# Performance work log

Measured on AMD Instinct MI355X. Metric: run time of the kernel, lower is better.

## Reference

```python
import jax, jax.numpy as jnp
import numpy as np
from jax import lax

GROUP = 4  # rt_group_size, reflection=False


def build_weights(W):
    """Symmetrize per GConv3d.get_weight (mid layer, no reflection, no Hermitian).
    W: (O, 1, I, G, kY, kX, kT) -> (O*G, I*G, kY, kX, kT).
    Each group copy k is the previous copy rotated 90 deg in the (kY, kX) plane
    followed by a cyclic shift (+1) along the input-group axis.
    """
    base = W[:, 0]  # (O, I, G, kY, kX, kT)
    ws = [base]
    for _ in range(1, GROUP):
        r = jnp.rot90(ws[-1], k=1, axes=(-3, -2))
        ws.append(jnp.roll(r, shift=1, axis=2))  # cat([last, :-1]) on group axis
    w = jnp.stack(ws, axis=1)  # (O, G, I, G, kY, kX, kT)
    O, _, I, _, kY, kX, kT = w.shape
    return w.reshape(O * GROUP, I * GROUP, kY, kX, kT)


def setup_inputs() -> dict:
    key = jax.random.key(0)
    k1, k2, k3 = jax.random.split(key, 3)
    in_ch, out_ch, k, kT = 16, 16, 3, 3
    x = jax.random.normal(k1, (4, in_ch * GROUP, 32, 64, 64), dtype=jnp.float32)
    # kaiming-ish scale: fan_in = in_ch * GROUP * k * k * kT
    scale = 1.0 / np.sqrt(in_ch * GROUP * k * k * kT)
    W = jax.random.normal(k2, (out_ch, 1, in_ch, GROUP, k, k, kT), dtype=jnp.float32) * scale
    B = jax.random.normal(k3, (1, out_ch, 1, 1, 1), dtype=jnp.float32) * scale
    return {"x": x, "W": W, "B": B}


def reference(x, W, B):
    w = build_weights(W)  # (O*G, I*G, kY, kX, kT)
    y = lax.conv_general_dilated(
        x, w, window_strides=(1, 1, 1), padding='VALID',
        dimension_numbers=('NCDHW', 'OIDHW', 'NCDHW'))
    bias = jnp.repeat(B, GROUP, axis=1)  # repeat_interleave along channel dim
    return y + bias
```

## Files before the change

### kernel.cpp

```cpp
#include <hip/hip_runtime.h>
#include <hip/hip_bf16.h>


typedef __attribute__((ext_vector_type(8))) short bf16x8;
typedef __attribute__((ext_vector_type(4))) float f32x4;

__device__ __forceinline__ void gl_lds16(const void* g, void* l) {
    __builtin_amdgcn_global_load_lds(
        (const __attribute__((address_space(1))) unsigned int*)g,
        (__attribute__((address_space(3))) unsigned int*)l, 16, 0, 0);
}

__global__ __launch_bounds__(256) void build_wT(const float* __restrict__ W,
                                                __hip_bfloat16* __restrict__ wT) {
    int idx = blockIdx.x * 256 + threadIdx.x;
    if (idx >= 27 * 64 * 64) return;
    int ic = idx & 63;
    int oc = (idx >> 6) & 63;
    int tap = idx >> 12;
    int kt = tap % 3, kx = (tap / 3) % 3, ky = tap / 9;
    int o = oc >> 2, kc = oc & 3, i = ic >> 2, gs = ic & 3;
    int sy = ky, sx = kx;
    for (int t = 0; t < kc; ++t) {
        int ny = sx, nx = 2 - sy;
        sy = ny; sx = nx;
        gs = (gs + 3) & 3;
    }
    wT[idx] = __float2bfloat16(W[((o * 16 + i) * 4 + gs) * 27 + sy * 9 + sx * 3 + kt]);
}

__device__ __forceinline__ unsigned int pack2(float a, float b) {
    union { __hip_bfloat162 h2; unsigned int u; } c;
    c.h2 = __hip_bfloat162{__float2bfloat16(a), __float2bfloat16(b)};
    return c.u;
}

__global__ __launch_bounds__(256) void transpose_x(const float* __restrict__ x,
                                                   __hip_bfloat16* __restrict__ xT) {
    __shared__ unsigned int ls[64 * 37];
    int bid = blockIdx.x;
    int hq = bid & 7, d = (bid >> 3) & 31, nb = bid >> 8;
    int tid = threadIdx.x;
    int w4 = tid & 15;
    int kp = tid >> 4;

    for (int hi = 0; hi < 8; ++hi) {
        int h = hq * 8 + hi;
        float4 v0[2], v1[2];
#pragma unroll
        for (int r = 0; r < 2; ++r) {
            int p = r * 16 + kp;
            const float* src = x + ((((size_t)nb * 64 + 2 * p) * 32 + d) * 64 + h) * 64 + w4 * 4;
            v0[r] = *(const float4*)(src);
            v1[r] = *(const float4*)(src + 32 * 64 * 64);
        }
        __syncthreads();
#pragma unroll
        for (int r = 0; r < 2; ++r) {
            int p = r * 16 + kp;
            ls[(w4 * 4 + 0) * 37 + p] = pack2(v0[r].x, v1[r].x);
            ls[(w4 * 4 + 1) * 37 + p] = pack2(v0[r].y, v1[r].y);
            ls[(w4 * 4 + 2) * 37 + p] = pack2(v0[r].z, v1[r].z);
            ls[(w4 * 4 + 3) * 37 + p] = pack2(v0[r].w, v1[r].w);
        }
        __syncthreads();
        __hip_bfloat16* obase = xT + (((size_t)nb * 32 + d) * 64 + h) * 4096;
#pragma unroll
        for (int c = tid; c < 512; c += 256) {
            int ww = c >> 3, icc = c & 7;
            const unsigned int* q = ls + ww * 37 + icc * 4;
            uint4 v;
            v.x = q[0]; v.y = q[1]; v.z = q[2]; v.w = q[3];
            *(uint4*)(obase + ww * 64 + icc * 8) = v;
        }
    }
}

__global__ __launch_bounds__(256, 2) void conv_mfma(const __hip_bfloat16* __restrict__ xT,
                                                    const __hip_bfloat16* __restrict__ wT,
                                                    const float* __restrict__ Bp,
                                                    float* __restrict__ out) {
    __shared__ __align__(16) short sB[6 * 4096 + 128];
    __shared__ __align__(16) short sA[2 * 4096];

    int orig = blockIdx.x;
    int bid = (orig & 7) * 240 + (orig >> 3);
    int ht = bid % 16;
    int d  = (bid / 16) % 30;
    int nb = bid / 480;
    int h0 = ht * 4;

    int tid = threadIdx.x;
    int w = tid >> 6;
    int lane = tid & 63;
    int quad = lane >> 4, col = lane & 15;

    f32x4 acc[4][4];
#pragma unroll
    for (int mt = 0; mt < 4; ++mt)
#pragma unroll
        for (int nt = 0; nt < 4; ++nt) acc[mt][nt] = (f32x4)(0.0f);

    int srcl = ((lane >> 3) << 6) + (((lane & 7) ^ (lane >> 3)) << 3);

    const __hip_bfloat16* xb = xT + (size_t)nb * 8388608 + (size_t)d * 262144;

#pragma unroll
    for (int i = 0; i < 2; ++i) {
        int p = w * 2 + i;
        gl_lds16(wT + p * 512 + srcl, (char*)sA + p * 1024);
    }

    for (int ky = 0; ky < 3; ++ky) {
#pragma unroll
        for (int i = 0; i < 12; ++i) {
            int p = w + i * 4;
            int hh = h0 + (p >> 3);
            if (hh > 63) hh = 63;
            gl_lds16(xb + (size_t)ky * 262144 + hh * 4096 + (p & 7) * 512 + srcl,
                     (char*)sB + p * 1024);
        }
        __syncthreads();

#pragma unroll
        for (int t = 0; t < 9; ++t) {
            {
                const __hip_bfloat16* asrc = wT + (ky * 9 + t + 1) * 4096 + srcl;
                char* adst = (char*)sA + (((ky * 9 + t + 1) & 1) ? 8192 : 0);
#pragma unroll
                for (int i = 0; i < 2; ++i) {
                    int p = w * 2 + i;
                    gl_lds16(asrc + p * 512, adst + p * 1024);
                }
            }

            const int kt = t % 3, kx = t / 3;
            const short* aBase = sA + ((ky * 9 + t) & 1) * 4096;
            int wc = col + kt;
            const short* pb = sB + ((w + kx) * 64 + wc) * 64;
            int bswz = (quad * 8) ^ ((wc & 7) << 3);

#pragma unroll
            for (int ich = 0; ich < 2; ++ich) {
                bf16x8 af[4], bfr[4];
#pragma unroll
                for (int mt = 0; mt < 4; ++mt)
                    af[mt] = *(const bf16x8*)(aBase + col * 64 + mt * 1024
                                              + (((ich * 4 + quad) ^ (col & 7)) << 3));
#pragma unroll
                for (int nt = 0; nt < 4; ++nt)
                    bfr[nt] = *(const bf16x8*)(pb + ((ich * 32) ^ bswz) + nt * 1024);

                __builtin_amdgcn_s_setprio(1);
#pragma unroll
                for (int mt = 0; mt < 4; ++mt)
#pragma unroll
                    for (int nt = 0; nt < 4; ++nt)
                        acc[mt][nt] = __builtin_amdgcn_mfma_f32_16x16x32_bf16(
                            af[mt], bfr[nt], acc[mt][nt], 0, 0, 0);
                __builtin_amdgcn_s_setprio(0);
            }

            __syncthreads();
        }
    }

    int hrow = h0 + w;
    if (hrow < 62) {
#pragma unroll
        for (int mt = 0; mt < 4; ++mt) {
            float bias = Bp[mt * 4 + quad];
#pragma unroll
            for (int nt = 0; nt < 4; ++nt) {
                int wp = nt * 16 + col;
                if (wp < 62) {
#pragma unroll
                    for (int r = 0; r < 4; ++r) {
                        int oc = mt * 16 + quad * 4 + r;
                        out[(((size_t)nb * 64 + oc) * 30 + d) * 3844 + hrow * 62 + wp]
                            = acc[mt][nt][r] + bias;
                    }
                }
            }
        }
    }
}

extern "C" void kernel_launch(void* const* d_in, const int* in_sizes, int n_in,
                              void* d_out, int out_size, void* d_ws, size_t ws_size,
                              hipStream_t stream) {
    const float* x = (const float*)d_in[0];
    const float* W = (const float*)d_in[1];
    const float* Bp = (const float*)d_in[2];
    float* out = (float*)d_out;

    char* ws = (char*)d_ws;
    __hip_bfloat16* wT = (__hip_bfloat16*)ws;
    __hip_bfloat16* xT = (__hip_bfloat16*)(ws + 262144);

    build_wT<<<(27 * 64 * 64 + 255) / 256, 256, 0, stream>>>(W, wT);
    transpose_x<<<4 * 32 * 8, 256, 0, stream>>>(x, xT);
    conv_mfma<<<4 * 30 * 16, 256, 0, stream>>>(xT, wT, Bp, out);
}
```

Measured before the change: 338.0 us.

## Double-buffer input slabs in LDS, stream weights to registers, prefetch transpose rows

The conv kernel now keeps two LDS input slabs. It prefetches the next ky slab during the current ky's taps, spread over the first six taps, and drops the per-tap block barriers. Weight fragments are loaded straight from global memory into registers one tap ahead instead of being staged in LDS. The transpose kernel gets a three-slot register pipeline that loads rows two iterations ahead to overlap global reads with LDS packing. The cost is doubled LDS use, which caps the conv kernel at one block per CU (launch bounds lowered to 1), plus more register pressure and weight reads that rely on the cache hierarchy.

```diff
diff --git a/kernel.cpp b/kernel.cpp
--- a/kernel.cpp
+++ b/kernel.cpp
@@ -44,27 +44,33 @@
     int w4 = tid & 15;
     int kp = tid >> 4;
 
+    float4 a[3][2], b[3][2];
+#define LOADROW(s, hh) do {                                                          \
+    const float* s0_ = x + ((((size_t)nb * 64 + 2 * kp) * 32 + d) * 64 + (hh)) * 64 + w4 * 4;        \
+    const float* s1_ = x + ((((size_t)nb * 64 + 2 * (16 + kp)) * 32 + d) * 64 + (hh)) * 64 + w4 * 4; \
+    a[s][0] = *(const float4*)s0_; b[s][0] = *(const float4*)(s0_ + 131072);         \
+    a[s][1] = *(const float4*)s1_; b[s][1] = *(const float4*)(s1_ + 131072);         \
+} while (0)
+
+    LOADROW(0, hq * 8 + 0);
+    LOADROW(1, hq * 8 + 1);
+#pragma unroll
     for (int hi = 0; hi < 8; ++hi) {
-        int h = hq * 8 + hi;
-        float4 v0[2], v1[2];
+        const int sc = hi % 3, sn = (hi + 2) % 3;
+        asm volatile("s_waitcnt lgkmcnt(0)" ::: "memory");
+        __builtin_amdgcn_s_barrier();
+        if (hi < 6) LOADROW(sn, hq * 8 + hi + 2);
 #pragma unroll
         for (int r = 0; r < 2; ++r) {
             int p = r * 16 + kp;
-            const float* src = x + ((((size_t)nb * 64 + 2 * p) * 32 + d) * 64 + h) * 64 + w4 * 4;
-            v0[r] = *(const float4*)(src);
-            v1[r] = *(const float4*)(src + 32 * 64 * 64);
-        }
-        __syncthreads();
-#pragma unroll
-        for (int r = 0; r < 2; ++r) {
-            int p = r * 16 + kp;
-            ls[(w4 * 4 + 0) * 37 + p] = pack2(v0[r].x, v1[r].x);
-            ls[(w4 * 4 + 1) * 37 + p] = pack2(v0[r].y, v1[r].y);
-            ls[(w4 * 4 + 2) * 37 + p] = pack2(v0[r].z, v1[r].z);
-            ls[(w4 * 4 + 3) * 37 + p] = pack2(v0[r].w, v1[r].w);
-        }
-        __syncthreads();
-        __hip_bfloat16* obase = xT + (((size_t)nb * 32 + d) * 64 + h) * 4096;
+            ls[(w4 * 4 + 0) * 37 + p] = pack2(a[sc][r].x, b[sc][r].x);
+            ls[(w4 * 4 + 1) * 37 + p] = pack2(a[sc][r].y, b[sc][r].y);
+            ls[(w4 * 4 + 2) * 37 + p] = pack2(a[sc][r].z, b[sc][r].z);
+            ls[(w4 * 4 + 3) * 37 + p] = pack2(a[sc][r].w, b[sc][r].w);
+        }
+        asm volatile("s_waitcnt lgkmcnt(0)" ::: "memory");
+        __builtin_amdgcn_s_barrier();
+        __hip_bfloat16* obase = xT + (((size_t)nb * 32 + d) * 64 + (hq * 8 + hi)) * 4096;
 #pragma unroll
         for (int c = tid; c < 512; c += 256) {
             int ww = c >> 3, icc = c & 7;
@@ -74,14 +80,14 @@
             *(uint4*)(obase + ww * 64 + icc * 8) = v;
         }
     }
-}
-
-__global__ __launch_bounds__(256, 2) void conv_mfma(const __hip_bfloat16* __restrict__ xT,
+#undef LOADROW
+}
+
+__global__ __launch_bounds__(256, 1) void conv_mfma(const __hip_bfloat16* __restrict__ xT,
                                                     const __hip_bfloat16* __restrict__ wT,
                                                     const float* __restrict__ Bp,
                                                     float* __restrict__ out) {
-    __shared__ __align__(16) short sB[6 * 4096 + 128];
-    __shared__ __align__(16) short sA[2 * 4096];
+    __shared__ __align__(16) short sB[2][6 * 4096 + 128];
 
     int orig = blockIdx.x;
     int bid = (orig & 7) * 240 + (orig >> 3);
@@ -104,65 +110,71 @@
     int srcl = ((lane >> 3) << 6) + (((lane & 7) ^ (lane >> 3)) << 3);
 
     const __hip_bfloat16* xb = xT + (size_t)nb * 8388608 + (size_t)d * 262144;
-
-#pragma unroll
-    for (int i = 0; i < 2; ++i) {
-        int p = w * 2 + i;
-        gl_lds16(wT + p * 512 + srcl, (char*)sA + p * 1024);
-    }
+    const __hip_bfloat16* aT = wT + col * 64 + quad * 8;
+
+#pragma unroll
+    for (int i = 0; i < 12; ++i) {
+        int p = w + i * 4;
+        int hh = h0 + (p >> 3);
+        if (hh > 63) hh = 63;
+        gl_lds16(xb + hh * 4096 + (p & 7) * 512 + srcl, (char*)sB[0] + p * 1024);
+    }
+    bf16x8 afc[4][2], afn[4][2];
+#pragma unroll
+    for (int mt = 0; mt < 4; ++mt)
+#pragma unroll
+        for (int ich = 0; ich < 2; ++ich)
+            afc[mt][ich] = *(const bf16x8*)(aT + mt * 1024 + ich * 32);
+    __syncthreads();
 
     for (int ky = 0; ky < 3; ++ky) {
-#pragma unroll
-        for (int i = 0; i < 12; ++i) {
-            int p = w + i * 4;
-            int hh = h0 + (p >> 3);
-            if (hh > 63) hh = 63;
-            gl_lds16(xb + (size_t)ky * 262144 + hh * 4096 + (p & 7) * 512 + srcl,
-                     (char*)sB + p * 1024);
-        }
-        __syncthreads();
+        const short* sBc = sB[ky & 1];
+        char* sBn = (char*)sB[(ky + 1) & 1];
+        const __hip_bfloat16* xn = xb + (size_t)(ky + 1) * 262144;
 
 #pragma unroll
         for (int t = 0; t < 9; ++t) {
-            {
-                const __hip_bfloat16* asrc = wT + (ky * 9 + t + 1) * 4096 + srcl;
-                char* adst = (char*)sA + (((ky * 9 + t + 1) & 1) ? 8192 : 0);
+            int g = ky * 9 + t;
+#pragma unroll
+            for (int mt = 0; mt < 4; ++mt)
+#pragma unroll
+                for (int ich = 0; ich < 2; ++ich)
+                    afn[mt][ich] = *(const bf16x8*)(aT + (g + 1) * 4096
+                                                    + mt * 1024 + ich * 32);
+            if (ky < 2 && t < 6) {
 #pragma unroll
                 for (int i = 0; i < 2; ++i) {
-                    int p = w * 2 + i;
-                    gl_lds16(asrc + p * 512, adst + p * 1024);
+                    int p = w + (t * 2 + i) * 4;
+                    int hh = h0 + (p >> 3);
+                    if (hh > 63) hh = 63;
+                    gl_lds16(xn + hh * 4096 + (p & 7) * 512 + srcl, sBn + p * 1024);
                 }
             }
 
             const int kt = t % 3, kx = t / 3;
-            const short* aBase = sA + ((ky * 9 + t) & 1) * 4096;
             int wc = col + kt;
-            const short* pb = sB + ((w + kx) * 64 + wc) * 64;
+            const short* pb = sBc + ((w + kx) * 64 + wc) * 64;
             int bswz = (quad * 8) ^ ((wc & 7) << 3);
-
 #pragma unroll
             for (int ich = 0; ich < 2; ++ich) {
-                bf16x8 af[4], bfr[4];
-#pragma unroll
-                for (int mt = 0; mt < 4; ++mt)
-                    af[mt] = *(const bf16x8*)(aBase + col * 64 + mt * 1024
-                                              + (((ich * 4 + quad) ^ (col & 7)) << 3));
+                bf16x8 bfr[4];
 #pragma unroll
                 for (int nt = 0; nt < 4; ++nt)
                     bfr[nt] = *(const bf16x8*)(pb + ((ich * 32) ^ bswz) + nt * 1024);
-
-                __builtin_amdgcn_s_setprio(1);
 #pragma unroll
                 for (int mt = 0; mt < 4; ++mt)
 #pragma unroll
                     for (int nt = 0; nt < 4; ++nt)
                         acc[mt][nt] = __builtin_amdgcn_mfma_f32_16x16x32_bf16(
-                            af[mt], bfr[nt], acc[mt][nt], 0, 0, 0);
-                __builtin_amdgcn_s_setprio(0);
+                            afc[mt][ich], bfr[nt], acc[mt][nt], 0, 0, 0);
             }
-
-            __syncthreads();
-        }
+#pragma unroll
+            for (int mt = 0; mt < 4; ++mt)
+#pragma unroll
+                for (int ich = 0; ich < 2; ++ich)
+                    afc[mt][ich] = afn[mt][ich];
+        }
+        __syncthreads();
     }
 
     int hrow = h0 + w;
```

Result: slower. 492.3 us (+45.6%).
